# Kernel optimization log

Measured on AMD Instinct MI355X. Metric: run time of the kernel, lower is better.

The kernel has to match this reference:

```python
import jax, jax.numpy as jnp
import numpy as np
import math

FEATURE_DIM = 128
CLASS_NUM = 10000
BATCH = 4096


def setup_inputs() -> dict:
    key = jax.random.key(0)
    k1, k2, k3 = jax.random.split(key, 3)
    # feat scaled by 0.1 so squared distances are O(1) and exp(-d/1.8) is non-degenerate
    feat = jax.random.normal(k1, (BATCH, FEATURE_DIM), dtype=jnp.float32) * 0.1
    # xavier_uniform over [class_num, feature_dim]
    bound = math.sqrt(6.0 / (CLASS_NUM + FEATURE_DIM))
    weights = jax.random.uniform(k2, (CLASS_NUM, FEATURE_DIM), dtype=jnp.float32,
                                 minval=-bound, maxval=bound)
    label = jax.random.randint(k3, (BATCH,), 0, CLASS_NUM, dtype=jnp.int64)
    return {"feat": feat, "weights": weights, "label": label}


def reference(feat, weights, label):
    # pairwise squared euclidean distance via GEMM trick (avoids [B,C,D] diff tensor)
    f2 = jnp.sum(feat * feat, axis=-1, keepdims=True)          # [B,1]
    w2 = jnp.sum(weights * weights, axis=-1)[None, :]          # [1,C]
    metric = jnp.maximum(f2 + w2 - 2.0 * (feat @ weights.T), 0.0)  # [B,C]
    kernal_metric = jnp.exp(-metric / 1.8)                     # [B,C]
    # per-sample gather of the true-class kernel value; mean; clamp at 0.5
    cor = jnp.take_along_axis(kernal_metric, label[:, None].astype(jnp.int32), axis=1)[:, 0]
    avg = jnp.maximum(jnp.mean(cor), 0.5)
    # original uses .item() per sample -> scale is detached from the graph
    scale = jax.lax.stop_gradient(1.0 / avg) * math.log(CLASS_NUM - 1.0)
    return scale * kernal_metric
```

## Files before the change

kernel.cpp:

```cpp
#include <hip/hip_runtime.h>
#include <hip/hip_bf16.h>
#include <math.h>

#define FDIM  128
#define BATCH 4096
#define CNUM  10000

typedef __attribute__((ext_vector_type(8))) short short8;
typedef __attribute__((ext_vector_type(4))) float f32x4;

#define WS_FEATB 0
#define WS_WB    1048576
#define WS_F2    3608576
#define WS_W2    3624960
#define WS_COR   3664960

#define C2 0.80178372573096f

#define GL2LDS(g, l) __builtin_amdgcn_global_load_lds(                      \
    (const __attribute__((address_space(1))) void*)(g),                     \
    (__attribute__((address_space(3))) void*)(l), 16, 0, 0)

__global__ void prep_cor_kernel(const float* __restrict__ feat,
                                const float* __restrict__ weights,
                                const int* __restrict__ label,
                                __hip_bfloat16* __restrict__ featb,
                                __hip_bfloat16* __restrict__ wb,
                                float* __restrict__ f2,
                                float* __restrict__ w2,
                                float* __restrict__ cor) {
    int gw   = (blockIdx.x * blockDim.x + threadIdx.x) >> 6;
    int lane = threadIdx.x & 63;
    if (gw < BATCH + CNUM) {
        const float* src;
        __hip_bfloat16* dst;
        float* nrm;
        if (gw < BATCH) { src = feat    + (size_t)gw * FDIM; dst = featb + (size_t)gw * FDIM; nrm = f2 + gw; }
        else            { int r = gw - BATCH;
                          src = weights + (size_t)r  * FDIM; dst = wb    + (size_t)r  * FDIM; nrm = w2 + r; }
        float2 v = ((const float2*)src)[lane];
        __hip_bfloat162 b2;
        b2.x = __float2bfloat16(v.x);
        b2.y = __float2bfloat16(v.y);
        ((__hip_bfloat162*)dst)[lane] = b2;
        float ss = v.x * v.x + v.y * v.y;
        #pragma unroll
        for (int off = 32; off; off >>= 1) ss += __shfl_down(ss, off, 64);
        if (lane == 0) *nrm = ss;
    } else {
        int s = gw - (BATCH + CNUM);
        if (s >= BATCH) return;
        int lab = label[s];
        float2 f = ((const float2*)(feat    + (size_t)s   * FDIM))[lane];
        float2 w = ((const float2*)(weights + (size_t)lab * FDIM))[lane];
        float dx = f.x - w.x, dy = f.y - w.y;
        float ss = dx * dx + dy * dy;
        #pragma unroll
        for (int off = 32; off; off >>= 1) ss += __shfl_down(ss, off, 64);
        if (lane == 0) cor[s] = __expf(-ss * (1.0f / 1.8f));
    }
}

__launch_bounds__(512, 4)
__global__ void gemm_kernel(const __hip_bfloat16* __restrict__ featb,
                            const __hip_bfloat16* __restrict__ wb,
                            const float* __restrict__ f2,
                            const float* __restrict__ w2,
                            const float* __restrict__ cor,
                            float* __restrict__ out) {
    __shared__ __align__(16) char lds[65536];
    __shared__ float red[8];

    int bx   = blockIdx.x;
    int band = bx & 31;
    int cg   = bx >> 5;
    int tid  = threadIdx.x;
    int wid  = tid >> 6;
    int lane = tid & 63;
    int r16  = lane & 15;
    int kh   = lane >> 4;
    int aoff = (wid & 1) * 64;
    int boff = (wid >> 1) * 32;

    const char* Ab = (const char*)wb;

    #pragma unroll
    for (int p = 0; p < 4; ++p) {
        int idx = tid + p * 512;
        int row = idx >> 4, chk = idx & 15;
        int gc = cg * 128 + row; gc = gc < CNUM ? gc : CNUM - 1;
        GL2LDS(Ab + (size_t)gc * 256 + (chk ^ (row & 7)) * 16, lds + idx * 16);
    }

    {
        float s = 0.0f;
        #pragma unroll
        for (int i = 0; i < BATCH / 512; ++i) s += cor[tid + i * 512];
        #pragma unroll
        for (int off = 32; off; off >>= 1) s += __shfl_down(s, off, 64);
        if (lane == 0) red[wid] = s;
    }

    float f2n[2];
    #pragma unroll
    for (int n = 0; n < 2; ++n) f2n[n] = f2[band * 128 + boff + n * 16 + r16];

    __syncthreads();

    float tot = 0.0f;
    #pragma unroll
    for (int i = 0; i < 8; ++i) tot += red[i];
    float avg = fmaxf(tot * (1.0f / BATCH), 0.5f);
    float ls2 = log2f(logf((float)(CNUM - 1)) / avg);

    const char* Bb = (const char*)featb;
    short8 bfrag[4][2];
    #pragma unroll
    for (int kk = 0; kk < 4; ++kk)
        #pragma unroll
        for (int n = 0; n < 2; ++n) {
            int row = band * 128 + boff + n * 16 + r16;
            bfrag[kk][n] = *(const short8*)(Bb + (size_t)row * 256 + kk * 64 + kh * 16);
        }

    #pragma unroll
    for (int it = 0; it < 5; ++it) {
        int t   = it * 16 + cg;
        int cur = it & 1;

        if (it < 4) {
            int tn = t + 16;
            #pragma unroll
            for (int p = 0; p < 4; ++p) {
                int idx = tid + p * 512;
                int row = idx >> 4, chk = idx & 15;
                int gc = tn * 128 + row; gc = gc < CNUM ? gc : CNUM - 1;
                GL2LDS(Ab + (size_t)gc * 256 + (chk ^ (row & 7)) * 16,
                       lds + (cur ^ 1) * 32768 + idx * 16);
            }
        }
        __builtin_amdgcn_sched_barrier(0);

        const char* Abuf = lds + cur * 32768;
        f32x4 acc[4][2];
        #pragma unroll
        for (int m = 0; m < 4; ++m)
            #pragma unroll
            for (int n = 0; n < 2; ++n) acc[m][n] = (f32x4){0.f, 0.f, 0.f, 0.f};

        #pragma unroll
        for (int kk = 0; kk < 4; ++kk) {
            short8 a[4];
            #pragma unroll
            for (int m = 0; m < 4; ++m) {
                int row = aoff + m * 16 + r16;
                int c = (kk * 4 + kh) ^ (row & 7);
                a[m] = *(const short8*)(Abuf + row * 256 + c * 16);
            }
            #pragma unroll
            for (int m = 0; m < 4; ++m)
                #pragma unroll
                for (int n = 0; n < 2; ++n)
                    acc[m][n] = __builtin_amdgcn_mfma_f32_16x16x32_bf16(a[m], bfrag[kk][n], acc[m][n], 0, 0, 0);
        }

        int mbase = t * 128 + aoff;
        #pragma unroll
        for (int m = 0; m < 4; ++m) {
            int cm0 = mbase + m * 16 + kh * 4;
            bool ok = cm0 < CNUM;
            f32x4 w4 = *(const f32x4*)(w2 + (ok ? cm0 : 0));
            #pragma unroll
            for (int n = 0; n < 2; ++n) {
                f32x4 v;
                #pragma unroll
                for (int r = 0; r < 4; ++r) {
                    float mt2 = fmaf(-2.0f, acc[m][n][r], f2n[n] + w4[r]);
                    mt2 = fmaxf(mt2, 0.0f);
                    v[r] = exp2f(fmaf(mt2, -C2, ls2));
                }
                if (ok) {
                    size_t rg = (size_t)(band * 128 + boff + n * 16 + r16);
                    *(f32x4*)(out + rg * CNUM + cm0) = v;
                }
            }
        }

        asm volatile("s_waitcnt vmcnt(8)" ::: "memory");
        __builtin_amdgcn_sched_barrier(0);
        __builtin_amdgcn_s_barrier();
    }
}

extern "C" void kernel_launch(void* const* d_in, const int* in_sizes, int n_in,
                              void* d_out, int out_size, void* d_ws, size_t ws_size,
                              hipStream_t stream) {
    (void)in_sizes; (void)n_in; (void)out_size; (void)ws_size;
    const float* feat    = (const float*)d_in[0];
    const float* weights = (const float*)d_in[1];
    const int*   label   = (const int*)d_in[2];
    float* out = (float*)d_out;
    char*  ws  = (char*)d_ws;

    __hip_bfloat16* featb = (__hip_bfloat16*)(ws + WS_FEATB);
    __hip_bfloat16* wb    = (__hip_bfloat16*)(ws + WS_WB);
    float* f2  = (float*)(ws + WS_F2);
    float* w2  = (float*)(ws + WS_W2);
    float* cor = (float*)(ws + WS_COR);

    const int total_waves = BATCH + CNUM + BATCH;
    prep_cor_kernel<<<(total_waves + 3) / 4, 256, 0, stream>>>(
        feat, weights, label, featb, wb, f2, w2, cor);

    gemm_kernel<<<512, 512, 0, stream>>>(featb, wb, f2, w2, cor, out);
}
```

Before: 49.60 us.

## Give each block a contiguous class range, cache w2 in LDS, split MFMA epilogue

Each block now covers a contiguous range of 640 classes (5 tiles of 128) instead of tiles strided by 16, so its output writes per row are contiguous. The w2 norms for that range are preloaded into LDS, replacing per-tile global loads in the epilogue. The M loop is split into two halves so half the accumulators are finished and stored before the rest are computed, lowering register pressure and interleaving stores with MFMA work. Contiguous ranges can change the L2/HBM access pattern for the weight tiles, since neighbouring blocks no longer share strided tiles.

```diff
diff --git a/kernel.cpp b/kernel.cpp
--- a/kernel.cpp
+++ b/kernel.cpp
@@ -16,6 +16,8 @@
 #define WS_COR   3664960
 
 #define C2 0.80178372573096f
+
+#define CGCLS 640
 
 #define GL2LDS(g, l) __builtin_amdgcn_global_load_lds(                      \
     (const __attribute__((address_space(1))) void*)(g),                     \
@@ -69,6 +71,7 @@
                             const float* __restrict__ cor,
                             float* __restrict__ out) {
     __shared__ __align__(16) char lds[65536];
+    __shared__ __align__(16) float w2l[CGCLS];
     __shared__ float red[8];
 
     int bx   = blockIdx.x;
@@ -83,15 +86,15 @@
     int boff = (wid >> 1) * 32;
 
     const char* Ab = (const char*)wb;
+    const char* Bb = (const char*)featb;
 
     #pragma unroll
     for (int p = 0; p < 4; ++p) {
         int idx = tid + p * 512;
         int row = idx >> 4, chk = idx & 15;
-        int gc = cg * 128 + row; gc = gc < CNUM ? gc : CNUM - 1;
+        int gc = cg * CGCLS + row; gc = gc < CNUM ? gc : CNUM - 1;
         GL2LDS(Ab + (size_t)gc * 256 + (chk ^ (row & 7)) * 16, lds + idx * 16);
     }
-
     {
         float s = 0.0f;
         #pragma unroll
@@ -100,11 +103,24 @@
         for (int off = 32; off; off >>= 1) s += __shfl_down(s, off, 64);
         if (lane == 0) red[wid] = s;
     }
-
+    #pragma unroll
+    for (int p = 0; p < 2; ++p) {
+        int idx = tid + p * 512;
+        if (idx < CGCLS) {
+            int cls = cg * CGCLS + idx;
+            w2l[idx] = (cls < CNUM) ? w2[cls] : 0.0f;
+        }
+    }
     float f2n[2];
-    #pragma unroll
-    for (int n = 0; n < 2; ++n) f2n[n] = f2[band * 128 + boff + n * 16 + r16];
-
+    short8 bfrag[4][2];
+    #pragma unroll
+    for (int n = 0; n < 2; ++n) {
+        int rowg = band * 128 + boff + n * 16 + r16;
+        f2n[n] = f2[rowg];
+        #pragma unroll
+        for (int kk = 0; kk < 4; ++kk)
+            bfrag[kk][n] = *(const short8*)(Bb + (size_t)rowg * 256 + kk * 64 + kh * 16);
+    }
     __syncthreads();
 
     float tot = 0.0f;
@@ -113,28 +129,17 @@
     float avg = fmaxf(tot * (1.0f / BATCH), 0.5f);
     float ls2 = log2f(logf((float)(CNUM - 1)) / avg);
 
-    const char* Bb = (const char*)featb;
-    short8 bfrag[4][2];
-    #pragma unroll
-    for (int kk = 0; kk < 4; ++kk)
-        #pragma unroll
-        for (int n = 0; n < 2; ++n) {
-            int row = band * 128 + boff + n * 16 + r16;
-            bfrag[kk][n] = *(const short8*)(Bb + (size_t)row * 256 + kk * 64 + kh * 16);
-        }
-
     #pragma unroll
     for (int it = 0; it < 5; ++it) {
-        int t   = it * 16 + cg;
         int cur = it & 1;
 
         if (it < 4) {
-            int tn = t + 16;
             #pragma unroll
             for (int p = 0; p < 4; ++p) {
                 int idx = tid + p * 512;
                 int row = idx >> 4, chk = idx & 15;
-                int gc = tn * 128 + row; gc = gc < CNUM ? gc : CNUM - 1;
+                int gc = cg * CGCLS + (it + 1) * 128 + row;
+                gc = gc < CNUM ? gc : CNUM - 1;
                 GL2LDS(Ab + (size_t)gc * 256 + (chk ^ (row & 7)) * 16,
                        lds + (cur ^ 1) * 32768 + idx * 16);
             }
@@ -142,46 +147,52 @@
         __builtin_amdgcn_sched_barrier(0);
 
         const char* Abuf = lds + cur * 32768;
-        f32x4 acc[4][2];
-        #pragma unroll
-        for (int m = 0; m < 4; ++m)
-            #pragma unroll
-            for (int n = 0; n < 2; ++n) acc[m][n] = (f32x4){0.f, 0.f, 0.f, 0.f};
-
-        #pragma unroll
-        for (int kk = 0; kk < 4; ++kk) {
-            short8 a[4];
-            #pragma unroll
-            for (int m = 0; m < 4; ++m) {
-                int row = aoff + m * 16 + r16;
-                int c = (kk * 4 + kh) ^ (row & 7);
-                a[m] = *(const short8*)(Abuf + row * 256 + c * 16);
+
+        #pragma unroll
+        for (int mp = 0; mp < 2; ++mp) {
+            f32x4 acc[2][2];
+            #pragma unroll
+            for (int mm = 0; mm < 2; ++mm)
+                #pragma unroll
+                for (int n = 0; n < 2; ++n) acc[mm][n] = (f32x4){0.f, 0.f, 0.f, 0.f};
+
+            #pragma unroll
+            for (int kk = 0; kk < 4; ++kk) {
+                short8 a0, a1;
+                {
+                    int row0 = aoff + (mp * 2 + 0) * 16 + r16;
+                    int c0 = (kk * 4 + kh) ^ (row0 & 7);
+                    a0 = *(const short8*)(Abuf + row0 * 256 + c0 * 16);
+                    int row1 = aoff + (mp * 2 + 1) * 16 + r16;
+                    int c1 = (kk * 4 + kh) ^ (row1 & 7);
+                    a1 = *(const short8*)(Abuf + row1 * 256 + c1 * 16);
+                }
+                #pragma unroll
+                for (int n = 0; n < 2; ++n) {
+                    acc[0][n] = __builtin_amdgcn_mfma_f32_16x16x32_bf16(a0, bfrag[kk][n], acc[0][n], 0, 0, 0);
+                    acc[1][n] = __builtin_amdgcn_mfma_f32_16x16x32_bf16(a1, bfrag[kk][n], acc[1][n], 0, 0, 0);
+                }
             }
-            #pragma unroll
-            for (int m = 0; m < 4; ++m)
+
+            #pragma unroll
+            for (int mm = 0; mm < 2; ++mm) {
+                int lcl = it * 128 + aoff + (mp * 2 + mm) * 16 + kh * 4;
+                int cm0 = cg * CGCLS + lcl;
+                bool ok = cm0 < CNUM;
+                f32x4 w4 = *(const f32x4*)(&w2l[lcl]);
                 #pragma unroll
-                for (int n = 0; n < 2; ++n)
-                    acc[m][n] = __builtin_amdgcn_mfma_f32_16x16x32_bf16(a[m], bfrag[kk][n], acc[m][n], 0, 0, 0);
-        }
-
-        int mbase = t * 128 + aoff;
-        #pragma unroll
-        for (int m = 0; m < 4; ++m) {
-            int cm0 = mbase + m * 16 + kh * 4;
-            bool ok = cm0 < CNUM;
-            f32x4 w4 = *(const f32x4*)(w2 + (ok ? cm0 : 0));
-            #pragma unroll
-            for (int n = 0; n < 2; ++n) {
-                f32x4 v;
-                #pragma unroll
-                for (int r = 0; r < 4; ++r) {
-                    float mt2 = fmaf(-2.0f, acc[m][n][r], f2n[n] + w4[r]);
-                    mt2 = fmaxf(mt2, 0.0f);
-                    v[r] = exp2f(fmaf(mt2, -C2, ls2));
-                }
-                if (ok) {
-                    size_t rg = (size_t)(band * 128 + boff + n * 16 + r16);
-                    *(f32x4*)(out + rg * CNUM + cm0) = v;
+                for (int n = 0; n < 2; ++n) {
+                    f32x4 v;
+                    #pragma unroll
+                    for (int r = 0; r < 4; ++r) {
+                        float mt2 = fmaf(-2.0f, acc[mm][n][r], f2n[n] + w4[r]);
+                        mt2 = fmaxf(mt2, 0.0f);
+                        v[r] = exp2f(fmaf(mt2, -C2, ls2));
+                    }
+                    if (ok) {
+                        size_t rg = (size_t)(band * 128 + boff + n * 16 + r16);
+                        *(f32x4*)(out + rg * CNUM + cm0) = v;
+                    }
                 }
             }
         }
```

Result: faster. 47.49 us (-4.3%).
